# Kernel optimization log

Measured on AMD Instinct MI355X. Metric: run time of the kernel, lower is better.

Reference implementation:

```python
import jax, jax.numpy as jnp
import numpy as np

B, T, S, D, H, FF = 4, 1024, 1024, 1024, 16, 4096
DH = D // H
NEG = -1e9
EPS = 1e-5


def setup_inputs() -> dict:
    key = jax.random.key(0)
    ks = jax.random.split(key, 20)
    p = 0.02  # param init scale
    inp = {
        "x": jax.random.normal(ks[0], (B, T, D), jnp.float32),
        "encoder_output": jax.random.normal(ks[1], (B, S, D), jnp.float32),
        "src_mask": jnp.ones((B, 1, 1, S), jnp.bool_),
        "tgt_mask": jnp.tril(jnp.ones((1, 1, T, T), jnp.bool_)),  # causal
        # self-attention params
        "d_Wq": jax.random.normal(ks[2], (D, D)) * p, "d_bq": jnp.zeros((D,)),
        "d_Wk": jax.random.normal(ks[3], (D, D)) * p, "d_bk": jnp.zeros((D,)),
        "d_Wv": jax.random.normal(ks[4], (D, D)) * p, "d_bv": jnp.zeros((D,)),
        "d_Wo": jax.random.normal(ks[5], (D, D)) * p, "d_bo": jnp.zeros((D,)),
        # cross-attention params
        "e_Wq": jax.random.normal(ks[6], (D, D)) * p, "e_bq": jnp.zeros((D,)),
        "e_Wk": jax.random.normal(ks[7], (D, D)) * p, "e_bk": jnp.zeros((D,)),
        "e_Wv": jax.random.normal(ks[8], (D, D)) * p, "e_bv": jnp.zeros((D,)),
        "e_Wo": jax.random.normal(ks[9], (D, D)) * p, "e_bo": jnp.zeros((D,)),
        # FFN params
        "ff_W1": jax.random.normal(ks[10], (D, FF)) * p, "ff_b1": jnp.zeros((FF,)),
        "ff_W2": jax.random.normal(ks[11], (FF, D)) * p, "ff_b2": jnp.zeros((D,)),
        # layernorm params
        "ln1_g": jnp.ones((D,)), "ln1_b": jnp.zeros((D,)),
        "ln2_g": jnp.ones((D,)), "ln2_b": jnp.zeros((D,)),
        "ln3_g": jnp.ones((D,)), "ln3_b": jnp.zeros((D,)),
    }
    return inp


def _mha(xq, xkv, Wq, bq, Wk, bk, Wv, bv, Wo, bo, mask):
    b, tq = xq.shape[0], xq.shape[1]
    q = (xq @ Wq + bq).reshape(b, tq, H, DH).transpose(0, 2, 1, 3)
    k = (xkv @ Wk + bk).reshape(b, -1, H, DH).transpose(0, 2, 1, 3)
    v = (xkv @ Wv + bv).reshape(b, -1, H, DH).transpose(0, 2, 1, 3)
    scores = jnp.einsum("bhqd,bhkd->bhqk", q, k) / np.float32(np.sqrt(DH))
    scores = jnp.where(mask, scores, NEG)
    attn = jax.nn.softmax(scores, axis=-1)
    out = jnp.einsum("bhqk,bhkd->bhqd", attn, v)
    out = out.transpose(0, 2, 1, 3).reshape(b, tq, D)
    return out @ Wo + bo


def _ln(x, g, b):
    m = jnp.mean(x, axis=-1, keepdims=True)
    v = jnp.var(x, axis=-1, keepdims=True)
    return (x - m) / jnp.sqrt(v + EPS) * g + b


def reference(x, encoder_output, src_mask, tgt_mask,
              d_Wq, d_bq, d_Wk, d_bk, d_Wv, d_bv, d_Wo, d_bo,
              e_Wq, e_bq, e_Wk, e_bk, e_Wv, e_bv, e_Wo, e_bo,
              ff_W1, ff_b1, ff_W2, ff_b2,
              ln1_g, ln1_b, ln2_g, ln2_b, ln3_g, ln3_b):
    # masked self-attention + residual + LN (dropout is identity in eval)
    d = _mha(x, x, d_Wq, d_bq, d_Wk, d_bk, d_Wv, d_bv, d_Wo, d_bo, tgt_mask)
    d = _ln(d + x, ln1_g, ln1_b)
    # cross-attention over encoder output + residual + LN
    f = _mha(d, encoder_output, e_Wq, e_bq, e_Wk, e_bk, e_Wv, e_bv, e_Wo, e_bo, src_mask)
    f = _ln(f + d, ln2_g, ln2_b)
    # FFN + residual + LN
    g = jax.nn.relu(f @ ff_W1 + ff_b1) @ ff_W2 + ff_b2
    g = _ln(g + f, ln3_g, ln3_b)
    return g
```

## Files before the change

### kernel.cpp

```cpp
#include <hip/hip_runtime.h>

static constexpr int Bc = 4, Tc = 1024, Sc = 1024, Dc = 1024, Hc = 16, DHc = 64, FFc = 4096;

typedef __attribute__((ext_vector_type(8))) short short8;
typedef __attribute__((ext_vector_type(4))) short short4v;
typedef __attribute__((ext_vector_type(4))) float f32x4;

__device__ __forceinline__ unsigned short f2bf(float f) {
    unsigned int u = __float_as_uint(f);
    unsigned int r = u + 0x7fffu + ((u >> 16) & 1u);
    return (unsigned short)(r >> 16);
}
__device__ __forceinline__ float bf2f(unsigned short u) {
    return __uint_as_float(((unsigned int)u) << 16);
}

__device__ __forceinline__ void gload_lds16(const void* g, void* l) {
    __builtin_amdgcn_global_load_lds((const __attribute__((address_space(1))) void*)g,
                                     (__attribute__((address_space(3))) void*)l, 16, 0, 0);
}

__global__ __launch_bounds__(256) void cast_f32_bf16(const float* __restrict__ in,
                                                     unsigned short* __restrict__ out, int n8) {
    int i = blockIdx.x * 256 + threadIdx.x;
    if (i >= n8) return;
    const float4* p = (const float4*)in + (size_t)i * 2;
    float4 a = p[0], b = p[1];
    short8 o;
    o[0] = f2bf(a.x); o[1] = f2bf(a.y); o[2] = f2bf(a.z); o[3] = f2bf(a.w);
    o[4] = f2bf(b.x); o[5] = f2bf(b.y); o[6] = f2bf(b.z); o[7] = f2bf(b.w);
    *(short8*)(out + (size_t)i * 8) = o;
}

__global__ __launch_bounds__(256) void transpose_cast(const float* __restrict__ W,
                                                      unsigned short* __restrict__ Wt,
                                                      int K, int N) {
    __shared__ float tile[32][33];
    int n0 = blockIdx.x * 32, k0 = blockIdx.y * 32;
    int tx = threadIdx.x, ty = threadIdx.y;
#pragma unroll
    for (int i = 0; i < 4; i++)
        tile[ty + i * 8][tx] = W[(size_t)(k0 + ty + i * 8) * N + n0 + tx];
    __syncthreads();
#pragma unroll
    for (int i = 0; i < 4; i++)
        Wt[(size_t)(n0 + ty + i * 8) * K + k0 + tx] = f2bf(tile[tx][ty + i * 8]);
}

struct TP8 { const float* s[8]; unsigned short* d[8]; };
__global__ __launch_bounds__(256) void transpose_cast8(TP8 p) {
    __shared__ float tile[32][33];
    const float* W = p.s[blockIdx.z];
    unsigned short* Wt = p.d[blockIdx.z];
    int n0 = blockIdx.x * 32, k0 = blockIdx.y * 32;
    int tx = threadIdx.x, ty = threadIdx.y;
#pragma unroll
    for (int i = 0; i < 4; i++)
        tile[ty + i * 8][tx] = W[(size_t)(k0 + ty + i * 8) * 1024 + n0 + tx];
    __syncthreads();
#pragma unroll
    for (int i = 0; i < 4; i++)
        Wt[(size_t)(n0 + ty + i * 8) * 1024 + k0 + tx] = f2bf(tile[tx][ty + i * 8]);
}

__global__ void concat_bias(const float* b0, const float* b1, const float* b2,
                            float* __restrict__ out) {
    int i = blockIdx.x * 256 + threadIdx.x;
    int seg = i >> 10, j = i & 1023;
    const float* p = seg == 0 ? b0 : (seg == 1 ? b1 : b2);
    out[i] = p[j];
}

__global__ __launch_bounds__(256) void transpose_v(const unsigned short* __restrict__ V, int ldv,
                                                   unsigned short* __restrict__ Vt) {
    __shared__ unsigned short t[64 * 64];
    const int bh = blockIdx.y, b = bh >> 4, h = bh & 15;
    const int s0 = blockIdx.x * 64;
    const int tid = threadIdx.x;
    const int r = tid >> 2, ch = tid & 3;
    const unsigned short* src = V + (size_t)(b * 1024 + s0 + r) * ldv + h * 64 + ch * 16;
    short8 v0 = *(const short8*)src;
    short8 v1 = *(const short8*)(src + 8);
    int pw_ = (ch ^ r ^ (r >> 4)) & 3;
    *(short8*)(t + r * 64 + pw_ * 16) = v0;
    *(short8*)(t + r * 64 + pw_ * 16 + 8) = v1;
    __syncthreads();
    const int dh = tid >> 2, sc = (tid & 3) * 16;
    short8 o0, o1;
#pragma unroll
    for (int j = 0; j < 8; j++) {
        int c0 = sc + j, c1 = sc + 8 + j;
        o0[j] = t[c0 * 64 + (((dh >> 4) ^ c0 ^ (c0 >> 4)) & 3) * 16 + (dh & 15)];
        o1[j] = t[c1 * 64 + (((dh >> 4) ^ c1 ^ (c1 >> 4)) & 3) * 16 + (dh & 15)];
    }
    unsigned short* dst = Vt + ((size_t)bh * 64 + dh) * 1024 + s0 + sc;
    *(short8*)dst = o0;
    *(short8*)(dst + 8) = o1;
}

struct BlkMap { int m, n, z; };
__device__ __forceinline__ BlkMap remap_block() {
    const int gx = gridDim.x, gy = gridDim.y;
    const int nxy = gx * gy;
    const int nwg = nxy * gridDim.z;
    const int flat = (blockIdx.z * gy + blockIdx.y) * gx + blockIdx.x;
    const int id = (flat & 7) * (nwg >> 3) + (flat >> 3);
    const int pz = id / nxy;
    const int rz = id - pz * nxy;
    const int gwsh = (gx & 7) ? 2 : 3;
    const int gw = 1 << gwsh;
    const int gsz = gw * gy;
    const int grp = rz / gsz;
    const int rem = rz - grp * gsz;
    BlkMap r;
    r.m = rem >> gwsh;
    r.n = (grp << gwsh) + (rem & (gw - 1));
    r.z = pz;
    return r;
}

template <int EPI>
__global__ __launch_bounds__(512, 2) void gemm256(const unsigned short* __restrict__ A,
                                                  const unsigned short* __restrict__ Bt,
                                                  const float* __restrict__ bias,
                                                  unsigned short* __restrict__ outB,
                                                  int N, int lda, int ldb, int nk) {
    __shared__ unsigned short sm[4][16384];
    const int tid = threadIdx.x;
    const int lane = tid & 63, wid = tid >> 6;
    const int l4 = lane & 15, g = lane >> 4;
    const int wr = wid >> 2, wc = wid & 3;
    BlkMap bm = remap_block();
    const int m0 = bm.m * 256, n0 = bm.n * 256;
    const int srow = tid >> 3;
    const int schunk = (tid & 7) ^ (srow & 7);
    const int sw = l4 & 7;

    auto stA = [&](int sb, int seg, int k0) {
        gload_lds16(A + (size_t)(m0 + seg * 64 + srow) * lda + k0 + schunk * 8,
                    (char*)sm[sb] + seg * 8192 + tid * 16);
    };
    auto stB = [&](int sb, int seg, int k0) {
        gload_lds16(Bt + (size_t)(n0 + seg * 64 + srow) * ldb + k0 + schunk * 8,
                    (char*)sm[2 + sb] + seg * 8192 + tid * 16);
    };

    f32x4 acc[8][4] = {};
#pragma unroll
    for (int s = 0; s < 4; s++) stB(0, s, 0);
#pragma unroll
    for (int s = 0; s < 4; s++) stA(0, s, 0);
    asm volatile("s_waitcnt vmcnt(0)" ::: "memory");
    __builtin_amdgcn_s_barrier();

    for (int t = 0; t < nk; ++t) {
        const int bufR = t & 1, bufW = bufR ^ 1;
        const int kn = (t + 1) * 64;
        const bool pf = (t + 1 < nk);
        const unsigned short* As_ = sm[bufR];
        const unsigned short* Bs_ = sm[2 + bufR];
        short8 a[4], b0[4], b1[4];
        if (pf) { stB(bufW, 0, kn); stB(bufW, 1, kn); }
#pragma unroll
        for (int n = 0; n < 4; n++)
            b0[n] = *(const short8*)(Bs_ + (wc * 64 + n * 16 + l4) * 64 + (g ^ sw) * 8);
#pragma unroll
        for (int m = 0; m < 4; m++)
            a[m] = *(const short8*)(As_ + (wr * 128 + m * 16 + l4) * 64 + (g ^ sw) * 8);
        __builtin_amdgcn_s_barrier();
        __builtin_amdgcn_s_setprio(1);
#pragma unroll
        for (int m = 0; m < 4; m++)
#pragma unroll
            for (int n = 0; n < 4; n++)
                acc[m][n] = __builtin_amdgcn_mfma_f32_16x16x32_bf16(a[m], b0[n], acc[m][n], 0, 0, 0);
        __builtin_amdgcn_s_setprio(0);
        __builtin_amdgcn_s_barrier();
        if (pf) { stB(bufW, 2, kn); stB(bufW, 3, kn); }
#pragma unroll
        for (int n = 0; n < 4; n++)
            b1[n] = *(const short8*)(Bs_ + (wc * 64 + n * 16 + l4) * 64 + ((4 + g) ^ sw) * 8);
#pragma unroll
        for (int m = 0; m < 4; m++)
            a[m] = *(const short8*)(As_ + (wr * 128 + m * 16 + l4) * 64 + ((4 + g) ^ sw) * 8);
        __builtin_amdgcn_s_barrier();
        __builtin_amdgcn_s_setprio(1);
#pragma unroll
        for (int m = 0; m < 4; m++)
#pragma unroll
            for (int n = 0; n < 4; n++)
                acc[m][n] = __builtin_amdgcn_mfma_f32_16x16x32_bf16(a[m], b1[n], acc[m][n], 0, 0, 0);
        __builtin_amdgcn_s_setprio(0);
        if (pf) asm volatile("s_waitcnt vmcnt(4)" ::: "memory");
        else    asm volatile("s_waitcnt vmcnt(0)" ::: "memory");
        __builtin_amdgcn_s_barrier();
        if (pf) { stA(bufW, 0, kn); stA(bufW, 2, kn); }
#pragma unroll
        for (int m = 0; m < 4; m++)
            a[m] = *(const short8*)(As_ + (wr * 128 + 64 + m * 16 + l4) * 64 + (g ^ sw) * 8);
        __builtin_amdgcn_s_barrier();
        __builtin_amdgcn_s_setprio(1);
#pragma unroll
        for (int m = 0; m < 4; m++)
#pragma unroll
            for (int n = 0; n < 4; n++)
                acc[4 + m][n] = __builtin_amdgcn_mfma_f32_16x16x32_bf16(a[m], b0[n], acc[4 + m][n], 0, 0, 0);
        __builtin_amdgcn_s_setprio(0);
        __builtin_amdgcn_s_barrier();
        if (pf) { stA(bufW, 1, kn); stA(bufW, 3, kn); }
#pragma unroll
        for (int m = 0; m < 4; m++)
            a[m] = *(const short8*)(As_ + (wr * 128 + 64 + m * 16 + l4) * 64 + ((4 + g) ^ sw) * 8);
        __builtin_amdgcn_s_barrier();
        __builtin_amdgcn_s_setprio(1);
#pragma unroll
        for (int m = 0; m < 4; m++)
#pragma unroll
            for (int n = 0; n < 4; n++)
                acc[4 + m][n] = __builtin_amdgcn_mfma_f32_16x16x32_bf16(a[m], b1[n], acc[4 + m][n], 0, 0, 0);
        __builtin_amdgcn_s_setprio(0);
        if (pf) asm volatile("s_waitcnt vmcnt(2)" ::: "memory");
        __builtin_amdgcn_s_barrier();
    }
    const int rowB = m0 + wr * 128 + g * 4;
    const int colB = n0 + wc * 64 + l4;
#pragma unroll
    for (int n = 0; n < 4; n++) {
        float bv = bias[colB + n * 16];
#pragma unroll
        for (int m = 0; m < 8; m++) {
#pragma unroll
            for (int r = 0; r < 4; r++) {
                float v = acc[m][n][r] + bv;
                if (EPI == 2) v = fmaxf(v, 0.f);
                outB[(size_t)(rowB + m * 16 + r) * N + colB + n * 16] = f2bf(v);
            }
        }
    }
}

template <int EPI>
__global__ __launch_bounds__(256) void gemm_db(const unsigned short* __restrict__ A,
                                               const unsigned short* __restrict__ Bt,
                                               const float* __restrict__ bias,
                                               float* __restrict__ outF,
                                               unsigned short* __restrict__ outB,
                                               int M, int N, int Kloop, int lda, int ldb) {
    __shared__ unsigned short As[3][128 * 32];
    __shared__ unsigned short Bs[3][128 * 32];
    const int tid = threadIdx.x;
    const int w = tid >> 6, lane = tid & 63, l4 = lane & 15, g = lane >> 4;
    BlkMap bm = remap_block();
    const int m0 = bm.m * 128, n0 = bm.n * 128, z = bm.z;
    A += (size_t)z * Kloop;
    Bt += (size_t)z * Kloop;
    const int wr = w >> 1, wc = w & 1;
    f32x4 acc[4][4] = {};
    const int r0 = tid >> 2;
    const int kk = ((tid & 3) ^ ((tid >> 3) & 3)) * 8;
    const int sk = (l4 >> 1) & 3;
    const unsigned short* Ar0 = A + (size_t)(m0 + r0) * lda + kk;
    const unsigned short* Ar1 = A + (size_t)(m0 + 64 + r0) * lda + kk;
    const unsigned short* Br0 = Bt + (size_t)(n0 + r0) * ldb + kk;
    const unsigned short* Br1 = Bt + (size_t)(n0 + 64 + r0) * ldb + kk;
    auto stage = [&](int sb, int k0) {
        gload_lds16(Ar0 + k0, (char*)As[sb] + tid * 16);
        gload_lds16(Ar1 + k0, (char*)As[sb] + 4096 + tid * 16);
        gload_lds16(Br0 + k0, (char*)Bs[sb] + tid * 16);
        gload_lds16(Br1 + k0, (char*)Bs[sb] + 4096 + tid * 16);
    };
    const int nk = Kloop >> 5;
    stage(0, 0);
    stage(1, 32);
    asm volatile("s_waitcnt vmcnt(4)" ::: "memory");
    __builtin_amdgcn_s_barrier();
    asm volatile("" ::: "memory");
    int buf = 0;
    for (int t = 0; t < nk; ++t) {
        if (t + 2 < nk) {
            int b2 = buf + 2; if (b2 >= 3) b2 -= 3;
            stage(b2, (t + 2) * 32);
        }
        short8 a[4], b[4];
#pragma unroll
        for (int m = 0; m < 4; m++)
            a[m] = *(const short8*)(As[buf] + (wr * 64 + m * 16 + l4) * 32 + (g ^ sk) * 8);
#pragma unroll
        for (int n = 0; n < 4; n++)
            b[n] = *(const short8*)(Bs[buf] + (wc * 64 + n * 16 + l4) * 32 + (g ^ sk) * 8);
#pragma unroll
        for (int m = 0; m < 4; m++)
#pragma unroll
            for (int n = 0; n < 4; n++)
                acc[m][n] = __builtin_amdgcn_mfma_f32_16x16x32_bf16(a[m], b[n], acc[m][n], 0, 0, 0);
        if (t + 1 < nk) {
            if (t + 2 < nk) asm volatile("s_waitcnt vmcnt(4)" ::: "memory");
            else            asm volatile("s_waitcnt vmcnt(0)" ::: "memory");
            __builtin_amdgcn_s_barrier();
            asm volatile("" ::: "memory");
        }
        buf = (buf + 1 == 3) ? 0 : buf + 1;
    }
    const int rowB = m0 + wr * 64 + g * 4;
    const int colB = n0 + wc * 64 + l4;
    float* oF = (EPI == 1) ? outF + (size_t)z * M * N : outF;
#pragma unroll
    for (int n = 0; n < 4; n++) {
        float bv = (EPI == 1 && z != 0) ? 0.f : bias[colB + n * 16];
#pragma unroll
        for (int m = 0; m < 4; m++) {
#pragma unroll
            for (int r = 0; r < 4; r++) {
                float v = acc[m][n][r] + bv;
                if (EPI == 2) v = fmaxf(v, 0.f);
                size_t idx = (size_t)(rowB + m * 16 + r) * N + colB + n * 16;
                if (EPI == 1) oF[idx] = v;
                else outB[idx] = f2bf(v);
            }
        }
    }
}

template <int EPI>
__global__ __launch_bounds__(256) void gemm64_db(const unsigned short* __restrict__ A,
                                                 const unsigned short* __restrict__ Bt,
                                                 const float* __restrict__ bias,
                                                 float* __restrict__ outF,
                                                 unsigned short* __restrict__ outB,
                                                 int M, int N, int Kloop, int lda, int ldb) {
    __shared__ unsigned short As[3][64 * 32];
    __shared__ unsigned short Bs[3][128 * 32];
    const int tid = threadIdx.x;
    const int w = tid >> 6, lane = tid & 63, l4 = lane & 15, g = lane >> 4;
    BlkMap bm = remap_block();
    const int m0 = bm.m * 64, n0 = bm.n * 128;
    f32x4 acc[4][2] = {};
    const int r0 = tid >> 2;
    const int kk = ((tid & 3) ^ ((tid >> 3) & 3)) * 8;
    const int sk = (l4 >> 1) & 3;
    const unsigned short* Ar0 = A + (size_t)(m0 + r0) * lda + kk;
    const unsigned short* Br0 = Bt + (size_t)(n0 + r0) * ldb + kk;
    const unsigned short* Br1 = Bt + (size_t)(n0 + 64 + r0) * ldb + kk;
    auto stage = [&](int sb, int k0) {
        gload_lds16(Ar0 + k0, (char*)As[sb] + tid * 16);
        gload_lds16(Br0 + k0, (char*)Bs[sb] + tid * 16);
        gload_lds16(Br1 + k0, (char*)Bs[sb] + 4096 + tid * 16);
    };
    const int nk = Kloop >> 5;
    stage(0, 0);
    stage(1, 32);
    asm volatile("s_waitcnt vmcnt(3)" ::: "memory");
    __builtin_amdgcn_s_barrier();
    asm volatile("" ::: "memory");
    int buf = 0;
    for (int t = 0; t < nk; ++t) {
        if (t + 2 < nk) {
            int b2 = buf + 2; if (b2 >= 3) b2 -= 3;
            stage(b2, (t + 2) * 32);
        }
        short8 a[4], b[2];
#pragma unroll
        for (int m = 0; m < 4; m++)
            a[m] = *(const short8*)(As[buf] + (m * 16 + l4) * 32 + (g ^ sk) * 8);
#pragma unroll
        for (int n = 0; n < 2; n++)
            b[n] = *(const short8*)(Bs[buf] + (w * 32 + n * 16 + l4) * 32 + (g ^ sk) * 8);
#pragma unroll
        for (int m = 0; m < 4; m++)
#pragma unroll
            for (int n = 0; n < 2; n++)
                acc[m][n] = __builtin_amdgcn_mfma_f32_16x16x32_bf16(a[m], b[n], acc[m][n], 0, 0, 0);
        if (t + 1 < nk) {
            if (t + 2 < nk) asm volatile("s_waitcnt vmcnt(3)" ::: "memory");
            else            asm volatile("s_waitcnt vmcnt(0)" ::: "memory");
            __builtin_amdgcn_s_barrier();
            asm volatile("" ::: "memory");
        }
        buf = (buf + 1 == 3) ? 0 : buf + 1;
    }
    const int rowB = m0 + g * 4;
    const int colB = n0 + w * 32 + l4;
#pragma unroll
    for (int n = 0; n < 2; n++) {
        float bv = bias[colB + n * 16];
#pragma unroll
        for (int m = 0; m < 4; m++) {
#pragma unroll
            for (int r = 0; r < 4; r++) {
                float v = acc[m][n][r] + bv;
                if (EPI == 2) v = fmaxf(v, 0.f);
                size_t idx = (size_t)(rowB + m * 16 + r) * N + colB + n * 16;
                if (EPI == 1) outF[idx] = v;
                else outB[idx] = f2bf(v);
            }
        }
    }
}

template <int CAUSAL>
__global__ __launch_bounds__(256) void attn4_kernel(const unsigned short* __restrict__ Q, int ldq,
                                                    const unsigned short* __restrict__ Kg, int ldk,
                                                    const unsigned short* __restrict__ Vt,
                                                    unsigned short* __restrict__ O) {
    __shared__ unsigned short Kl[2 * 64 * 64];
    __shared__ unsigned short Vl[2 * 64 * 64];
    __shared__ unsigned short Pl[4][16 * 72];
    const int bh = blockIdx.x, qb = blockIdx.y;
    const int b = bh >> 4, h = bh & 15;
    const int tid = threadIdx.x, w = tid >> 6, lane = tid & 63;
    const int l4 = lane & 15, g = lane >> 4;
    const int q0 = qb * 64 + w * 16;
    const unsigned short* Qp = Q + (size_t)(b * Tc + q0 + l4) * ldq + h * DHc + g * 8;
    short8 qf0 = *(const short8*)Qp;
    short8 qf1 = *(const short8*)(Qp + 32);
    const unsigned short* Kbase = Kg + (size_t)(b * 1024) * ldk + h * DHc;
    const unsigned short* Vbase = Vt + (size_t)bh * DHc * 1024;
    f32x4 o[4] = {};
    float mrun = -1e30f, lrun = 0.f;
    const int nT = CAUSAL ? qb + 1 : 16;
    unsigned short* pw = &Pl[w][l4 * 72];
    const int qi = q0 + l4;

    const int sr0 = tid >> 3;
    const int sr1 = 32 + sr0;
    const int sc_ = (tid & 7) ^ (sr0 & 7);

    auto stage = [&](int s0, int buf) {
        char* kd = (char*)Kl + buf * 8192;
        char* vd = (char*)Vl + buf * 8192;
        gload_lds16(Kbase + (size_t)(s0 + sr0) * ldk + sc_ * 8, kd + tid * 16);
        gload_lds16(Kbase + (size_t)(s0 + sr1) * ldk + sc_ * 8, kd + 4096 + tid * 16);
        gload_lds16(Vbase + (size_t)sr0 * 1024 + s0 + sc_ * 8, vd + tid * 16);
        gload_lds16(Vbase + (size_t)sr1 * 1024 + s0 + sc_ * 8, vd + 4096 + tid * 16);
    };

    stage(0, 0);
    __syncthreads();
    int buf = 0;
    const int sw = l4 & 7;

    for (int t = 0; t < nT; ++t) {
        const int s0 = t * 64;
        if (t + 1 < nT) stage(s0 + 64, buf ^ 1);
        const unsigned short* Kb_ = Kl + buf * 4096;
        const unsigned short* Vb_ = Vl + buf * 4096;
        f32x4 st[4];
        f32x4 z = {0.f, 0.f, 0.f, 0.f};
        __builtin_amdgcn_s_setprio(1);
#pragma unroll
        for (int c = 0; c < 4; c++) {
            const unsigned short* kr = Kb_ + (c * 16 + l4) * 64;
            short8 ka0 = *(const short8*)(kr + ((g ^ sw) * 8));
            short8 ka1 = *(const short8*)(kr + (((g + 4) ^ sw) * 8));
            st[c] = __builtin_amdgcn_mfma_f32_16x16x32_bf16(ka0, qf0, z, 0, 0, 0);
            st[c] = __builtin_amdgcn_mfma_f32_16x16x32_bf16(ka1, qf1, st[c], 0, 0, 0);
        }
        __builtin_amdgcn_s_setprio(0);
        float p[16];
        float tmax = -1e30f;
        const bool domask = CAUSAL && (t == nT - 1);
#pragma unroll
        for (int c = 0; c < 4; c++)
#pragma unroll
            for (int r = 0; r < 4; r++) {
                float v = st[c][r] * 0.125f;
                if (domask && (s0 + c * 16 + g * 4 + r) > qi) v = -1e9f;
                p[c * 4 + r] = v;
                tmax = fmaxf(tmax, v);
            }
        tmax = fmaxf(tmax, __shfl_xor(tmax, 16));
        tmax = fmaxf(tmax, __shfl_xor(tmax, 32));
        if (!__all(tmax <= mrun + 8.f)) {
            float mnew = fmaxf(mrun, tmax);
            float al = __expf(mrun - mnew);
            lrun *= al;
#pragma unroll
            for (int d = 0; d < 4; d++) o[d] *= al;
            mrun = mnew;
        }
        float ps = 0.f;
#pragma unroll
        for (int i = 0; i < 16; i++) { p[i] = __expf(p[i] - mrun); ps += p[i]; }
        ps += __shfl_xor(ps, 16);
        ps += __shfl_xor(ps, 32);
        lrun += ps;
#pragma unroll
        for (int c = 0; c < 4; c++) {
            short4v pk;
            pk[0] = f2bf(p[c * 4 + 0]); pk[1] = f2bf(p[c * 4 + 1]);
            pk[2] = f2bf(p[c * 4 + 2]); pk[3] = f2bf(p[c * 4 + 3]);
            *(short4v*)(pw + c * 16 + g * 4) = pk;
        }
        short8 pb_lo = *(const short8*)(pw + g * 8);
        short8 pb_hi = *(const short8*)(pw + 32 + g * 8);
        __builtin_amdgcn_s_setprio(1);
#pragma unroll
        for (int d = 0; d < 4; d++) {
            const unsigned short* vr = Vb_ + (d * 16 + l4) * 64;
            short8 va0 = *(const short8*)(vr + ((g ^ sw) * 8));
            short8 va1 = *(const short8*)(vr + (((g + 4) ^ sw) * 8));
            o[d] = __builtin_amdgcn_mfma_f32_16x16x32_bf16(va0, pb_lo, o[d], 0, 0, 0);
            o[d] = __builtin_amdgcn_mfma_f32_16x16x32_bf16(va1, pb_hi, o[d], 0, 0, 0);
        }
        __builtin_amdgcn_s_setprio(0);
        __syncthreads();
        buf ^= 1;
    }
    float inv = 1.f / lrun;
    unsigned short* Ob = O + (size_t)(b * Tc + q0 + l4) * Dc + h * DHc;
#pragma unroll
    for (int d = 0; d < 4; d++) {
#pragma unroll
        for (int r = 0; r < 4; r++) Ob[d * 16 + g * 4 + r] = f2bf(o[d][r] * inv);
    }
}

__global__ __launch_bounds__(256) void ln_bf(const unsigned short* __restrict__ a,
                                             const unsigned short* __restrict__ res,
                                             const float* __restrict__ gam,
                                             const float* __restrict__ bet,
                                             unsigned short* __restrict__ outB,
                                             float* __restrict__ outF) {
    int row = blockIdx.x, t = threadIdx.x;
    size_t base = (size_t)row * Dc + t * 4;
    short4v av = *(const short4v*)(a + base);
    short4v rv = *(const short4v*)(res + base);
    float x0 = bf2f((unsigned short)av[0]) + bf2f((unsigned short)rv[0]);
    float x1 = bf2f((unsigned short)av[1]) + bf2f((unsigned short)rv[1]);
    float x2 = bf2f((unsigned short)av[2]) + bf2f((unsigned short)rv[2]);
    float x3 = bf2f((unsigned short)av[3]) + bf2f((unsigned short)rv[3]);
    float s = x0 + x1 + x2 + x3;
    float ss = x0 * x0 + x1 * x1 + x2 * x2 + x3 * x3;
    for (int o = 1; o < 64; o <<= 1) { s += __shfl_xor(s, o); ss += __shfl_xor(ss, o); }
    __shared__ float S1[4], S2[4];
    int w = t >> 6;
    if ((t & 63) == 0) { S1[w] = s; S2[w] = ss; }
    __syncthreads();
    s = S1[0] + S1[1] + S1[2] + S1[3];
    ss = S2[0] + S2[1] + S2[2] + S2[3];
    float mean = s * (1.f / Dc);
    float var = ss * (1.f / Dc) - mean * mean;
    float rstd = rsqrtf(var + 1e-5f);
    int c = t * 4;
    float4 g4 = *(const float4*)(gam + c);
    float4 b4 = *(const float4*)(bet + c);
    float y0 = (x0 - mean) * rstd * g4.x + b4.x;
    float y1 = (x1 - mean) * rstd * g4.y + b4.y;
    float y2 = (x2 - mean) * rstd * g4.z + b4.z;
    float y3 = (x3 - mean) * rstd * g4.w + b4.w;
    if (outB) {
        short4v ob;
        ob[0] = f2bf(y0); ob[1] = f2bf(y1); ob[2] = f2bf(y2); ob[3] = f2bf(y3);
        *(short4v*)(outB + base) = ob;
    }
    if (outF) { float4 ov = {y0, y1, y2, y3}; *(float4*)(outF + base) = ov; }
}

__global__ __launch_bounds__(256) void ln_2f(const float* __restrict__ a0,
                                             const float* __restrict__ a1,
                                             const unsigned short* __restrict__ res,
                                             const float* __restrict__ gam,
                                             const float* __restrict__ bet,
                                             unsigned short* __restrict__ outB,
                                             float* __restrict__ outF) {
    int row = blockIdx.x, t = threadIdx.x;
    size_t base = (size_t)row * Dc + t * 4;
    float4 u = *(const float4*)(a0 + base);
    float4 v = *(const float4*)(a1 + base);
    short4v rv = *(const short4v*)(res + base);
    float x0 = u.x + v.x + bf2f((unsigned short)rv[0]);
    float x1 = u.y + v.y + bf2f((unsigned short)rv[1]);
    float x2 = u.z + v.z + bf2f((unsigned short)rv[2]);
    float x3 = u.w + v.w + bf2f((unsigned short)rv[3]);
    float s = x0 + x1 + x2 + x3;
    float ss = x0 * x0 + x1 * x1 + x2 * x2 + x3 * x3;
    for (int o = 1; o < 64; o <<= 1) { s += __shfl_xor(s, o); ss += __shfl_xor(ss, o); }
    __shared__ float S1[4], S2[4];
    int w = t >> 6;
    if ((t & 63) == 0) { S1[w] = s; S2[w] = ss; }
    __syncthreads();
    s = S1[0] + S1[1] + S1[2] + S1[3];
    ss = S2[0] + S2[1] + S2[2] + S2[3];
    float mean = s * (1.f / Dc);
    float var = ss * (1.f / Dc) - mean * mean;
    float rstd = rsqrtf(var + 1e-5f);
    int c = t * 4;
    float4 g4 = *(const float4*)(gam + c);
    float4 b4 = *(const float4*)(bet + c);
    float y0 = (x0 - mean) * rstd * g4.x + b4.x;
    float y1 = (x1 - mean) * rstd * g4.y + b4.y;
    float y2 = (x2 - mean) * rstd * g4.z + b4.z;
    float y3 = (x3 - mean) * rstd * g4.w + b4.w;
    if (outB) {
        short4v ob;
        ob[0] = f2bf(y0); ob[1] = f2bf(y1); ob[2] = f2bf(y2); ob[3] = f2bf(y3);
        *(short4v*)(outB + base) = ob;
    }
    if (outF) { float4 ov = {y0, y1, y2, y3}; *(float4*)(outF + base) = ov; }
}

extern "C" void kernel_launch(void* const* d_in, const int* in_sizes, int n_in,
                              void* d_out, int out_size, void* d_ws, size_t ws_size,
                              hipStream_t stream) {
    const float* x   = (const float*)d_in[0];
    const float* enc = (const float*)d_in[1];
    const float* dWq = (const float*)d_in[4];  const float* dbq = (const float*)d_in[5];
    const float* dWk = (const float*)d_in[6];  const float* dbk = (const float*)d_in[7];
    const float* dWv = (const float*)d_in[8];  const float* dbv = (const float*)d_in[9];
    const float* dWo = (const float*)d_in[10]; const float* dbo = (const float*)d_in[11];
    const float* eWq = (const float*)d_in[12]; const float* ebq = (const float*)d_in[13];
    const float* eWk = (const float*)d_in[14]; const float* ebk = (const float*)d_in[15];
    const float* eWv = (const float*)d_in[16]; const float* ebv = (const float*)d_in[17];
    const float* eWo = (const float*)d_in[18]; const float* ebo = (const float*)d_in[19];
    const float* fW1 = (const float*)d_in[20]; const float* fb1 = (const float*)d_in[21];
    const float* fW2 = (const float*)d_in[22]; const float* fb2 = (const float*)d_in[23];
    const float* g1 = (const float*)d_in[24];  const float* be1 = (const float*)d_in[25];
    const float* g2 = (const float*)d_in[26];  const float* be2 = (const float*)d_in[27];
    const float* g3 = (const float*)d_in[28];  const float* be3 = (const float*)d_in[29];

    char* ws = (char*)d_ws;
    size_t off = 0;
    auto alloc = [&](size_t bytes) -> void* {
        void* p = ws + off;
        off += (bytes + 255) & ~(size_t)255;
        return p;
    };
    const size_t A = (size_t)4096 * 1024;
    const size_t MB1 = (size_t)1024 * 1024;
    char* R1 = (char*)alloc(32 * 1024 * 1024);
    unsigned short* qkv = (unsigned short*)R1;
    unsigned short* kvx = (unsigned short*)R1;
    unsigned short* qx  = (unsigned short*)(R1 + 16 * 1024 * 1024);
    unsigned short* h1  = (unsigned short*)R1;
    unsigned short* xb   = (unsigned short*)alloc(A * 2);
    unsigned short* encb = (unsigned short*)alloc(A * 2);
    unsigned short* wqkv = (unsigned short*)alloc(3 * MB1 * 2);
    unsigned short* wekv = (unsigned short*)alloc(2 * MB1 * 2);
    unsigned short* weq  = (unsigned short*)alloc(MB1 * 2);
    unsigned short* wdo  = (unsigned short*)alloc(MB1 * 2);
    unsigned short* weo  = (unsigned short*)alloc(MB1 * 2);
    unsigned short* wf1  = (unsigned short*)alloc(4 * MB1 * 2);
    unsigned short* wf2  = (unsigned short*)alloc(4 * MB1 * 2);
    float* bqkv = (float*)alloc(3072 * 4);
    float* bekv = (float*)alloc(2048 * 4);
    unsigned short* VtB = (unsigned short*)alloc(A * 2);
    unsigned short* ab  = (unsigned short*)alloc(A * 2);
    unsigned short* tmpB = (unsigned short*)alloc(A * 2);
    unsigned short* dB = (unsigned short*)alloc(A * 2);
    unsigned short* fB = (unsigned short*)alloc(A * 2);
    float* pf0 = (float*)VtB;
    float* pf1 = pf0 + A;
    (void)ws_size; (void)in_sizes; (void)n_in; (void)out_size;

    dim3 tb(32, 8);
    cast_f32_bf16<<<2048, 256, 0, stream>>>(x, xb, (int)(A / 8));
    cast_f32_bf16<<<2048, 256, 0, stream>>>(enc, encb, (int)(A / 8));
    TP8 tp;
    tp.s[0] = dWq; tp.d[0] = wqkv;
    tp.s[1] = dWk; tp.d[1] = wqkv + MB1;
    tp.s[2] = dWv; tp.d[2] = wqkv + 2 * MB1;
    tp.s[3] = eWk; tp.d[3] = wekv;
    tp.s[4] = eWv; tp.d[4] = wekv + MB1;
    tp.s[5] = eWq; tp.d[5] = weq;
    tp.s[6] = dWo; tp.d[6] = wdo;
    tp.s[7] = eWo; tp.d[7] = weo;
    transpose_cast8<<<dim3(32, 32, 8), tb, 0, stream>>>(tp);
    transpose_cast<<<dim3(128, 32), tb, 0, stream>>>(fW1, wf1, 1024, 4096);
    transpose_cast<<<dim3(32, 128), tb, 0, stream>>>(fW2, wf2, 4096, 1024);
    concat_bias<<<12, 256, 0, stream>>>(dbq, dbk, dbv, bqkv);
    concat_bias<<<8, 256, 0, stream>>>(ebk, ebv, ebv, bekv);

    gemm256<0><<<dim3(12, 16), 512, 0, stream>>>(xb, wqkv, bqkv, qkv, 3072, 1024, 1024, 16);
    transpose_v<<<dim3(16, 64), 256, 0, stream>>>(qkv + 2048, 3072, VtB);
    attn4_kernel<1><<<dim3(64, 16), 256, 0, stream>>>(qkv, 3072, qkv + 1024, 3072, VtB, ab);
    gemm64_db<0><<<dim3(8, 64), 256, 0, stream>>>(ab, wdo, dbo, nullptr, tmpB, 4096, 1024, 1024, 1024, 1024);
    ln_bf<<<4096, 256, 0, stream>>>(tmpB, xb, g1, be1, dB, nullptr);

    gemm_db<0><<<dim3(16, 32, 1), 256, 0, stream>>>(encb, wekv, bekv, nullptr, kvx, 4096, 2048, 1024, 1024, 1024);
    gemm64_db<0><<<dim3(8, 64), 256, 0, stream>>>(dB, weq, ebq, nullptr, qx, 4096, 1024, 1024, 1024, 1024);
    transpose_v<<<dim3(16, 64), 256, 0, stream>>>(kvx + 1024, 2048, VtB);
    attn4_kernel<0><<<dim3(64, 16), 256, 0, stream>>>(qx, 1024, kvx, 2048, VtB, ab);
    gemm64_db<0><<<dim3(8, 64), 256, 0, stream>>>(ab, weo, ebo, nullptr, tmpB, 4096, 1024, 1024, 1024, 1024);
    ln_bf<<<4096, 256, 0, stream>>>(tmpB, dB, g2, be2, fB, nullptr);

    gemm256<2><<<dim3(16, 16), 512, 0, stream>>>(fB, wf1, fb1, h1, 4096, 1024, 1024, 16);
    gemm_db<1><<<dim3(8, 32, 2), 256, 0, stream>>>(h1, wf2, fb2, pf0, nullptr, 4096, 1024, 2048, 4096, 4096);
    ln_2f<<<4096, 256, 0, stream>>>(pf0, pf1, fB, g3, be3, nullptr, (float*)d_out);
}
```

Measured before the change: 363.1 us.

## Route cross-attn KV and FFN2 GEMMs through 256-tile kernel with bf16 split-K

Removes the 128-tile gemm_db kernel. The cross-attention K/V projection now runs on the 256x256 gemm256 kernel. FFN2 now uses gemm256 with a 4-way split-K that writes bf16 partials, and a new layernorm kernel sums the four partials with the residual. This gives the larger-tile kernel more data reuse and halves partial-sum traffic compared with fp32 partials. In exchange, the KV GEMM launches only 128 blocks, which may underfill the GPU, and rounding the partial sums to bf16 adds precision error before the final layernorm.

```diff
diff --git a/kernel.cpp b/kernel.cpp
--- a/kernel.cpp
+++ b/kernel.cpp
@@ -131,7 +131,9 @@
     const int l4 = lane & 15, g = lane >> 4;
     const int wr = wid >> 2, wc = wid & 3;
     BlkMap bm = remap_block();
-    const int m0 = bm.m * 256, n0 = bm.n * 256;
+    const int m0 = bm.m * 256, n0 = bm.n * 256, z = bm.z;
+    A += (size_t)z * (nk * 64);
+    Bt += (size_t)z * (nk * 64);
     const int srow = tid >> 3;
     const int schunk = (tid & 7) ^ (srow & 7);
     const int sw = l4 & 7;
@@ -224,98 +226,18 @@
     }
     const int rowB = m0 + wr * 128 + g * 4;
     const int colB = n0 + wc * 64 + l4;
+    unsigned short* oB = outB;
+    if (EPI == 3) oB += (size_t)z * ((size_t)gridDim.y * 256) * N;
 #pragma unroll
     for (int n = 0; n < 4; n++) {
-        float bv = bias[colB + n * 16];
+        float bv = (EPI == 3 && z != 0) ? 0.f : bias[colB + n * 16];
 #pragma unroll
         for (int m = 0; m < 8; m++) {
 #pragma unroll
             for (int r = 0; r < 4; r++) {
                 float v = acc[m][n][r] + bv;
                 if (EPI == 2) v = fmaxf(v, 0.f);
-                outB[(size_t)(rowB + m * 16 + r) * N + colB + n * 16] = f2bf(v);
-            }
-        }
-    }
-}
-
-template <int EPI>
-__global__ __launch_bounds__(256) void gemm_db(const unsigned short* __restrict__ A,
-                                               const unsigned short* __restrict__ Bt,
-                                               const float* __restrict__ bias,
-                                               float* __restrict__ outF,
-                                               unsigned short* __restrict__ outB,
-                                               int M, int N, int Kloop, int lda, int ldb) {
-    __shared__ unsigned short As[3][128 * 32];
-    __shared__ unsigned short Bs[3][128 * 32];
-    const int tid = threadIdx.x;
-    const int w = tid >> 6, lane = tid & 63, l4 = lane & 15, g = lane >> 4;
-    BlkMap bm = remap_block();
-    const int m0 = bm.m * 128, n0 = bm.n * 128, z = bm.z;
-    A += (size_t)z * Kloop;
-    Bt += (size_t)z * Kloop;
-    const int wr = w >> 1, wc = w & 1;
-    f32x4 acc[4][4] = {};
-    const int r0 = tid >> 2;
-    const int kk = ((tid & 3) ^ ((tid >> 3) & 3)) * 8;
-    const int sk = (l4 >> 1) & 3;
-    const unsigned short* Ar0 = A + (size_t)(m0 + r0) * lda + kk;
-    const unsigned short* Ar1 = A + (size_t)(m0 + 64 + r0) * lda + kk;
-    const unsigned short* Br0 = Bt + (size_t)(n0 + r0) * ldb + kk;
-    const unsigned short* Br1 = Bt + (size_t)(n0 + 64 + r0) * ldb + kk;
-    auto stage = [&](int sb, int k0) {
-        gload_lds16(Ar0 + k0, (char*)As[sb] + tid * 16);
-        gload_lds16(Ar1 + k0, (char*)As[sb] + 4096 + tid * 16);
-        gload_lds16(Br0 + k0, (char*)Bs[sb] + tid * 16);
-        gload_lds16(Br1 + k0, (char*)Bs[sb] + 4096 + tid * 16);
-    };
-    const int nk = Kloop >> 5;
-    stage(0, 0);
-    stage(1, 32);
-    asm volatile("s_waitcnt vmcnt(4)" ::: "memory");
-    __builtin_amdgcn_s_barrier();
-    asm volatile("" ::: "memory");
-    int buf = 0;
-    for (int t = 0; t < nk; ++t) {
-        if (t + 2 < nk) {
-            int b2 = buf + 2; if (b2 >= 3) b2 -= 3;
-            stage(b2, (t + 2) * 32);
-        }
-        short8 a[4], b[4];
-#pragma unroll
-        for (int m = 0; m < 4; m++)
-            a[m] = *(const short8*)(As[buf] + (wr * 64 + m * 16 + l4) * 32 + (g ^ sk) * 8);
-#pragma unroll
-        for (int n = 0; n < 4; n++)
-            b[n] = *(const short8*)(Bs[buf] + (wc * 64 + n * 16 + l4) * 32 + (g ^ sk) * 8);
-#pragma unroll
-        for (int m = 0; m < 4; m++)
-#pragma unroll
-            for (int n = 0; n < 4; n++)
-                acc[m][n] = __builtin_amdgcn_mfma_f32_16x16x32_bf16(a[m], b[n], acc[m][n], 0, 0, 0);
-        if (t + 1 < nk) {
-            if (t + 2 < nk) asm volatile("s_waitcnt vmcnt(4)" ::: "memory");
-            else            asm volatile("s_waitcnt vmcnt(0)" ::: "memory");
-            __builtin_amdgcn_s_barrier();
-            asm volatile("" ::: "memory");
-        }
-        buf = (buf + 1 == 3) ? 0 : buf + 1;
-    }
-    const int rowB = m0 + wr * 64 + g * 4;
-    const int colB = n0 + wc * 64 + l4;
-    float* oF = (EPI == 1) ? outF + (size_t)z * M * N : outF;
-#pragma unroll
-    for (int n = 0; n < 4; n++) {
-        float bv = (EPI == 1 && z != 0) ? 0.f : bias[colB + n * 16];
-#pragma unroll
-        for (int m = 0; m < 4; m++) {
-#pragma unroll
-            for (int r = 0; r < 4; r++) {
-                float v = acc[m][n][r] + bv;
-                if (EPI == 2) v = fmaxf(v, 0.f);
-                size_t idx = (size_t)(rowB + m * 16 + r) * N + colB + n * 16;
-                if (EPI == 1) oF[idx] = v;
-                else outB[idx] = f2bf(v);
+                oB[(size_t)(rowB + m * 16 + r) * N + colB + n * 16] = f2bf(v);
             }
         }
     }
@@ -556,22 +478,26 @@
     if (outF) { float4 ov = {y0, y1, y2, y3}; *(float4*)(outF + base) = ov; }
 }
 
-__global__ __launch_bounds__(256) void ln_2f(const float* __restrict__ a0,
-                                             const float* __restrict__ a1,
+__global__ __launch_bounds__(256) void ln_4b(const unsigned short* __restrict__ p,
                                              const unsigned short* __restrict__ res,
                                              const float* __restrict__ gam,
                                              const float* __restrict__ bet,
-                                             unsigned short* __restrict__ outB,
                                              float* __restrict__ outF) {
+    const size_t PS = (size_t)4096 * 1024;
     int row = blockIdx.x, t = threadIdx.x;
     size_t base = (size_t)row * Dc + t * 4;
-    float4 u = *(const float4*)(a0 + base);
-    float4 v = *(const float4*)(a1 + base);
-    short4v rv = *(const short4v*)(res + base);
-    float x0 = u.x + v.x + bf2f((unsigned short)rv[0]);
-    float x1 = u.y + v.y + bf2f((unsigned short)rv[1]);
-    float x2 = u.z + v.z + bf2f((unsigned short)rv[2]);
-    float x3 = u.w + v.w + bf2f((unsigned short)rv[3]);
+    float x0, x1, x2, x3;
+    {
+        short4v rv = *(const short4v*)(res + base);
+        x0 = bf2f((unsigned short)rv[0]); x1 = bf2f((unsigned short)rv[1]);
+        x2 = bf2f((unsigned short)rv[2]); x3 = bf2f((unsigned short)rv[3]);
+    }
+#pragma unroll
+    for (int j = 0; j < 4; j++) {
+        short4v v = *(const short4v*)(p + j * PS + base);
+        x0 += bf2f((unsigned short)v[0]); x1 += bf2f((unsigned short)v[1]);
+        x2 += bf2f((unsigned short)v[2]); x3 += bf2f((unsigned short)v[3]);
+    }
     float s = x0 + x1 + x2 + x3;
     float ss = x0 * x0 + x1 * x1 + x2 * x2 + x3 * x3;
     for (int o = 1; o < 64; o <<= 1) { s += __shfl_xor(s, o); ss += __shfl_xor(ss, o); }
@@ -587,16 +513,12 @@
     int c = t * 4;
     float4 g4 = *(const float4*)(gam + c);
     float4 b4 = *(const float4*)(bet + c);
-    float y0 = (x0 - mean) * rstd * g4.x + b4.x;
-    float y1 = (x1 - mean) * rstd * g4.y + b4.y;
-    float y2 = (x2 - mean) * rstd * g4.z + b4.z;
-    float y3 = (x3 - mean) * rstd * g4.w + b4.w;
-    if (outB) {
-        short4v ob;
-        ob[0] = f2bf(y0); ob[1] = f2bf(y1); ob[2] = f2bf(y2); ob[3] = f2bf(y3);
-        *(short4v*)(outB + base) = ob;
-    }
-    if (outF) { float4 ov = {y0, y1, y2, y3}; *(float4*)(outF + base) = ov; }
+    float4 ov;
+    ov.x = (x0 - mean) * rstd * g4.x + b4.x;
+    ov.y = (x1 - mean) * rstd * g4.y + b4.y;
+    ov.z = (x2 - mean) * rstd * g4.z + b4.z;
+    ov.w = (x3 - mean) * rstd * g4.w + b4.w;
+    *(float4*)(outF + base) = ov;
 }
 
 extern "C" void kernel_launch(void* const* d_in, const int* in_sizes, int n_in,
@@ -648,8 +570,7 @@
     unsigned short* tmpB = (unsigned short*)alloc(A * 2);
     unsigned short* dB = (unsigned short*)alloc(A * 2);
     unsigned short* fB = (unsigned short*)alloc(A * 2);
-    float* pf0 = (float*)VtB;
-    float* pf1 = pf0 + A;
+    unsigned short* pfb = VtB;
     (void)ws_size; (void)in_sizes; (void)n_in; (void)out_size;
 
     dim3 tb(32, 8);
@@ -676,7 +597,7 @@
     gemm64_db<0><<<dim3(8, 64), 256, 0, stream>>>(ab, wdo, dbo, nullptr, tmpB, 4096, 1024, 1024, 1024, 1024);
     ln_bf<<<4096, 256, 0, stream>>>(tmpB, xb, g1, be1, dB, nullptr);
 
-    gemm_db<0><<<dim3(16, 32, 1), 256, 0, stream>>>(encb, wekv, bekv, nullptr, kvx, 4096, 2048, 1024, 1024, 1024);
+    gemm256<0><<<dim3(8, 16), 512, 0, stream>>>(encb, wekv, bekv, kvx, 2048, 1024, 1024, 16);
     gemm64_db<0><<<dim3(8, 64), 256, 0, stream>>>(dB, weq, ebq, nullptr, qx, 4096, 1024, 1024, 1024, 1024);
     transpose_v<<<dim3(16, 64), 256, 0, stream>>>(kvx + 1024, 2048, VtB);
     attn4_kernel<0><<<dim3(64, 16), 256, 0, stream>>>(qx, 1024, kvx, 2048, VtB, ab);
@@ -684,6 +605,6 @@
     ln_bf<<<4096, 256, 0, stream>>>(tmpB, dB, g2, be2, fB, nullptr);
 
     gemm256<2><<<dim3(16, 16), 512, 0, stream>>>(fB, wf1, fb1, h1, 4096, 1024, 1024, 16);
-    gemm_db<1><<<dim3(8, 32, 2), 256, 0, stream>>>(h1, wf2, fb2, pf0, nullptr, 4096, 1024, 2048, 4096, 4096);
-    ln_2f<<<4096, 256, 0, stream>>>(pf0, pf1, fB, g3, be3, nullptr, (float*)d_out);
-}
+    gemm256<3><<<dim3(4, 16, 4), 512, 0, stream>>>(h1, wf2, fb2, pfb, 1024, 4096, 4096, 16);
+    ln_4b<<<4096, 256, 0, stream>>>(pfb, fB, g3, be3, (float*)d_out);
+}
```

Measured after the change: 364.1 us. About the same (+0.3%).
